# Kernel optimization log

Hardware: AMD Instinct MI355X
Metric: run time of the kernel (lower is better)

## Reference

```python
import jax, jax.numpy as jnp
import numpy as np

H = 32

def setup_inputs() -> dict:
    key = jax.random.key(0)
    ks = jax.random.split(key, 8)
    B, S = 256, 4096
    scale = 1.0 / np.sqrt(H)
    return {
        "lstm_outputs": jax.random.normal(ks[0], (B, S, H), dtype=jnp.float32),
        "final_hidden": jax.random.normal(ks[1], (B, H), dtype=jnp.float32),
        "Wq": jax.random.uniform(ks[2], (H, H), jnp.float32, -scale, scale),
        "bq": jax.random.uniform(ks[3], (H,), jnp.float32, -scale, scale),
        "Wk": jax.random.uniform(ks[4], (H, H), jnp.float32, -scale, scale),
        "bk": jax.random.uniform(ks[5], (H,), jnp.float32, -scale, scale),
        "Wv": jax.random.uniform(ks[6], (H, 1), jnp.float32, -scale, scale),
        "bv": jax.random.uniform(ks[7], (1,), jnp.float32, -scale, scale),
    }

def reference(lstm_outputs, final_hidden, Wq, bq, Wk, bk, Wv, bv):
    # keys: [B,S,H], query: [B,H]
    keys = jnp.einsum('bsh,hd->bsd', lstm_outputs, Wk) + bk
    query = final_hidden @ Wq + bq
    tanhed = jnp.tanh(query[:, None, :] + keys)            # [B,S,H]
    scores = jnp.einsum('bsh,h->bs', tanhed, Wv[:, 0]) + bv[0]  # [B,S]
    att_weights = jax.nn.softmax(scores, axis=-1)          # [B,S]
    context = jnp.einsum('bs,bsh->bh', att_weights, keys)  # [B,H]
    return context, att_weights
```

## Files before the change

kernel.cpp:

```cpp
#include <hip/hip_runtime.h>
#include <math.h>

#define HD 32
#define BB 256
#define SS 4096
#define BLK 256
#define POSB 256
#define NCH (SS / POSB)
#define PADW 40
#define PSTRIDE 33

typedef short bf16x8 __attribute__((ext_vector_type(8)));
typedef float f32x4 __attribute__((ext_vector_type(4)));

__device__ __forceinline__ float tanh_fast(float x) {
  float e = __builtin_amdgcn_exp2f(x * 2.8853900817779268f);
  return 1.0f - 2.0f * __builtin_amdgcn_rcpf(e + 1.0f);
}
__device__ __forceinline__ float exp_fast(float x) {
  return __builtin_amdgcn_exp2f(x * 1.4426950408889634f);
}
__device__ __forceinline__ short bf16_trunc(float x) {
  return (short)(__float_as_uint(x) >> 16);
}
__device__ __forceinline__ float hi_part(float x) {
  return __uint_as_float(__float_as_uint(x) & 0xffff0000u);
}
template <int CTRL>
__device__ __forceinline__ float dpp_ror(float x) {
  return __int_as_float(
      __builtin_amdgcn_update_dpp(0, __float_as_int(x), CTRL, 0xF, 0xF, true));
}

__global__ void __launch_bounds__(BLK, 4) bahdanau_p1(
    const float* __restrict__ lstm, const float* __restrict__ fh,
    const float* __restrict__ Wq, const float* __restrict__ bq,
    const float* __restrict__ Wk, const float* __restrict__ bk,
    const float* __restrict__ Wv, const float* __restrict__ bv,
    float* __restrict__ scores_out, float* __restrict__ partials) {
  __shared__ short sWkTh[HD * PADW];
  __shared__ short sWkTl[HD * PADW];
  __shared__ float sQB[HD];
  __shared__ float sWv[HD];
  __shared__ float sYp[4][HD];
  __shared__ float sRedL[4];

  const int tid = threadIdx.x;
  const int b = blockIdx.x >> 4;
  const int chunk = blockIdx.x & (NCH - 1);
  const int base = chunk * POSB;
  const int lane = tid & 63, w = tid >> 6;
  const int col = lane & 15, quad = lane >> 4;

  const float* gx = lstm + ((size_t)b * SS + base + w * 64) * HD;
  const float* rp = gx + (size_t)col * HD + quad * 8;
  float4 xa0 = ((const float4*)(rp + 0 * 16 * HD))[0];
  float4 xb0 = ((const float4*)(rp + 0 * 16 * HD))[1];
  float4 xa1 = ((const float4*)(rp + 1 * 16 * HD))[0];
  float4 xb1 = ((const float4*)(rp + 1 * 16 * HD))[1];
  float4 xa2 = ((const float4*)(rp + 2 * 16 * HD))[0];
  float4 xb2 = ((const float4*)(rp + 2 * 16 * HD))[1];
  float4 xa3 = ((const float4*)(rp + 3 * 16 * HD))[0];
  float4 xb3 = ((const float4*)(rp + 3 * 16 * HD))[1];

  {
    float4 w4 = ((const float4*)Wk)[tid];
    const int k = tid >> 3, h0 = (tid & 7) * 4;
    const float v[4] = {w4.x, w4.y, w4.z, w4.w};
#pragma unroll
    for (int i = 0; i < 4; i++) {
      const float hf = hi_part(v[i]);
      sWkTh[(h0 + i) * PADW + k] = bf16_trunc(v[i]);
      sWkTl[(h0 + i) * PADW + k] = bf16_trunc(v[i] - hf);
    }
  }
  if (tid < HD) {
    float acc = bq[tid] + bk[tid];
    const float* fhb = fh + b * HD;
#pragma unroll
    for (int j = 0; j < HD; j++) acc += fhb[j] * Wq[j * HD + tid];
    sQB[tid] = acc;
    sWv[tid] = Wv[tid];
  }
  __syncthreads();

  bf16x8 Bh0 = *(const bf16x8*)&sWkTh[(col)*PADW + quad * 8];
  bf16x8 Bl0 = *(const bf16x8*)&sWkTl[(col)*PADW + quad * 8];
  bf16x8 Bh1 = *(const bf16x8*)&sWkTh[(16 + col) * PADW + quad * 8];
  bf16x8 Bl1 = *(const bf16x8*)&sWkTl[(16 + col) * PADW + quad * 8];
  const float qb0 = sQB[col], qb1 = sQB[16 + col];
  const float wv0 = sWv[col], wv1 = sWv[16 + col];
  const float bv0 = bv[0];
  const int permLane = (col >> 2) * 16 + col;

  float lAcc = 0.f;
  float yp[8];
#pragma unroll
  for (int j = 0; j < 8; j++) yp[j] = 0.f;

#define MT_STEP(mt, XA, XB)                                                    \
  {                                                                            \
    const float xs[8] = {XA.x, XA.y, XA.z, XA.w, XB.x, XB.y, XB.z, XB.w};      \
    bf16x8 Ah, Al;                                                             \
    _Pragma("unroll") for (int j = 0; j < 8; j++) {                            \
      const float hf = hi_part(xs[j]);                                         \
      Ah[j] = bf16_trunc(xs[j]);                                               \
      Al[j] = bf16_trunc(xs[j] - hf);                                          \
    }                                                                          \
    f32x4 c0 = {0.f, 0.f, 0.f, 0.f}, c1 = {0.f, 0.f, 0.f, 0.f};                \
    c0 = __builtin_amdgcn_mfma_f32_16x16x32_bf16(Ah, Bh0, c0, 0, 0, 0);        \
    c1 = __builtin_amdgcn_mfma_f32_16x16x32_bf16(Ah, Bh1, c1, 0, 0, 0);        \
    c0 = __builtin_amdgcn_mfma_f32_16x16x32_bf16(Al, Bh0, c0, 0, 0, 0);        \
    c1 = __builtin_amdgcn_mfma_f32_16x16x32_bf16(Al, Bh1, c1, 0, 0, 0);        \
    c0 = __builtin_amdgcn_mfma_f32_16x16x32_bf16(Ah, Bl0, c0, 0, 0, 0);        \
    c1 = __builtin_amdgcn_mfma_f32_16x16x32_bf16(Ah, Bl1, c1, 0, 0, 0);        \
    float esc[4];                                                              \
    _Pragma("unroll") for (int r = 0; r < 4; r++) {                            \
      float t = tanh_fast(qb0 + c0[r]) * wv0 + tanh_fast(qb1 + c1[r]) * wv1;   \
      t += dpp_ror<0x128>(t);                                   \
      t += dpp_ror<0x124>(t);                                   \
      t += dpp_ror<0x122>(t);                                   \
      t += dpp_ror<0x121>(t);    \
      esc[r] = exp_fast(t + bv0);                                              \
    }                                                                          \
    const float s01 = (col & 1) ? esc[1] : esc[0];                             \
    const float s23 = (col & 1) ? esc[3] : esc[2];                             \
    const float sel = (col & 2) ? s23 : s01;        \
    const float e_m = __shfl(sel, permLane, 64);   \
    if (lane < 16)                                                             \
      scores_out[(size_t)b * SS + base + w * 64 + mt * 16 + lane] = e_m;       \
    lAcc += (lane < 16) ? e_m : 0.f;                                           \
    _Pragma("unroll") for (int j = 0; j < 8; j++)                              \
        yp[j] = fmaf(e_m, xs[j], yp[j]);                                       \
  }

  MT_STEP(0, xa0, xb0)
  MT_STEP(1, xa1, xb1)
  MT_STEP(2, xa2, xb2)
  MT_STEP(3, xa3, xb3)
#undef MT_STEP

#pragma unroll
  for (int j = 0; j < 8; j++) {
    yp[j] += __shfl_xor(yp[j], 1, 64);
    yp[j] += __shfl_xor(yp[j], 2, 64);
    yp[j] += __shfl_xor(yp[j], 4, 64);
    yp[j] += __shfl_xor(yp[j], 8, 64);
  }
  if (col == 0) {
#pragma unroll
    for (int j = 0; j < 8; j++) sYp[w][quad * 8 + j] = yp[j];
  }
#pragma unroll
  for (int off = 32; off >= 1; off >>= 1) lAcc += __shfl_xor(lAcc, off, 64);
  if (lane == 0) sRedL[w] = lAcc;
  __syncthreads();

  if (tid < HD) {
    float y = sYp[0][tid] + sYp[1][tid] + sYp[2][tid] + sYp[3][tid];
    float* p = partials + (size_t)blockIdx.x * PSTRIDE;
    p[1 + tid] = y;
    if (tid == 0) p[0] = sRedL[0] + sRedL[1] + sRedL[2] + sRedL[3];
  }
}

__global__ void __launch_bounds__(BLK) bahdanau_p2(
    const float* __restrict__ partials, const float* __restrict__ Wk,
    const float* __restrict__ bk, float* __restrict__ ctx_out,
    float* __restrict__ scores) {
  const int blk = blockIdx.x;
  const int b = blk >> 2;
  const int tid = threadIdx.x;
  __shared__ float sY[HD];

  float L = 0.f;
#pragma unroll
  for (int c = 0; c < NCH; c++)
    L += partials[(size_t)(b * NCH + c) * PSTRIDE];
  const float invL = __builtin_amdgcn_rcpf(L);

  if ((blk & 3) == 0) {
    if (tid < HD) {
      float y = 0.f;
#pragma unroll
      for (int c = 0; c < NCH; c++)
        y += partials[(size_t)(b * NCH + c) * PSTRIDE + 1 + tid];
      sY[tid] = y;
    }
    __syncthreads();
    if (tid < HD) {
      float cv = bk[tid] * L;
#pragma unroll
      for (int j = 0; j < HD; j++) cv = fmaf(sY[j], Wk[j * HD + tid], cv);
      ctx_out[b * HD + tid] = cv * invL;
    }
  }

  float4* srow = (float4*)(scores + (size_t)b * SS + (blk & 3) * 1024);
  float4 s = srow[tid];
  s.x *= invL; s.y *= invL; s.z *= invL; s.w *= invL;
  srow[tid] = s;
}

extern "C" void kernel_launch(void* const* d_in, const int* in_sizes, int n_in,
                              void* d_out, int out_size, void* d_ws,
                              size_t ws_size, hipStream_t stream) {
  const float* lstm = (const float*)d_in[0];
  const float* fh   = (const float*)d_in[1];
  const float* Wq   = (const float*)d_in[2];
  const float* bq   = (const float*)d_in[3];
  const float* Wk   = (const float*)d_in[4];
  const float* bk   = (const float*)d_in[5];
  const float* Wv   = (const float*)d_in[6];
  const float* bv   = (const float*)d_in[7];

  float* out = (float*)d_out;
  float* ctx_out = out;
  float* scores = out + BB * HD;
  float* partials = (float*)d_ws;

  bahdanau_p1<<<BB * NCH, BLK, 0, stream>>>(lstm, fh, Wq, bq, Wk, bk, Wv, bv,
                                            scores, partials);
  bahdanau_p2<<<BB * 4, BLK, 0, stream>>>(partials, Wk, bk, ctx_out, scores);
}
```

Before: 206.3 us.

## Hoist query/Wk split into prologue kernel, swap MFMA operands, per-wave partials

Adds a small prologue kernel that computes query+bias per batch and the bf16 hi/lo split of Wk once into workspace, so the main kernel no longer rebuilds them in LDS and needs no block barrier. The MFMA operands are swapped so that each lane holds per-position results over 4 hidden units. This lets the tanh/Wv reduction run as in-lane FMAs plus two cross-lane shuffles instead of DPP rotations and a permute shuffle. Each wave now writes its own partial record rather than reducing through shared memory, which makes the reduction kernel read 4x more partials. It also adds a third kernel launch.

Result: slower. 211.4 us (+2.4%).

```diff
diff --git a/kernel.cpp b/kernel.cpp
--- a/kernel.cpp
+++ b/kernel.cpp
@@ -7,8 +7,8 @@
 #define BLK 256
 #define POSB 256
 #define NCH (SS / POSB)
-#define PADW 40
-#define PSTRIDE 33
+#define NWREC 64
+#define PREC 36
 
 typedef short bf16x8 __attribute__((ext_vector_type(8)));
 typedef float f32x4 __attribute__((ext_vector_type(4)));
@@ -26,25 +26,39 @@
 __device__ __forceinline__ float hi_part(float x) {
   return __uint_as_float(__float_as_uint(x) & 0xffff0000u);
 }
-template <int CTRL>
-__device__ __forceinline__ float dpp_ror(float x) {
-  return __int_as_float(
-      __builtin_amdgcn_update_dpp(0, __float_as_int(x), CTRL, 0xF, 0xF, true));
+
+__global__ void __launch_bounds__(256) bahdanau_p0(
+    const float* __restrict__ fh, const float* __restrict__ Wq,
+    const float* __restrict__ bq, const float* __restrict__ bk,
+    const float* __restrict__ Wk, float* __restrict__ qbP,
+    short* __restrict__ wkH, short* __restrict__ wkL) {
+  const int tid = threadIdx.x;
+  if (blockIdx.x == 32) {
+    float4 w4 = ((const float4*)Wk)[tid];
+    const int k = tid >> 3, h0 = (tid & 7) * 4;
+    const float v[4] = {w4.x, w4.y, w4.z, w4.w};
+#pragma unroll
+    for (int i = 0; i < 4; i++) {
+      const float hf = hi_part(v[i]);
+      wkH[(h0 + i) * HD + k] = bf16_trunc(v[i]);
+      wkL[(h0 + i) * HD + k] = bf16_trunc(v[i] - hf);
+    }
+  } else {
+    const int b = blockIdx.x * 8 + (tid >> 5);
+    const int h = tid & 31;
+    float acc = bq[h] + bk[h];
+    const float* fhb = fh + b * HD;
+#pragma unroll
+    for (int j = 0; j < HD; j++) acc = fmaf(fhb[j], Wq[j * HD + h], acc);
+    qbP[b * HD + h] = acc;
+  }
 }
 
 __global__ void __launch_bounds__(BLK, 4) bahdanau_p1(
-    const float* __restrict__ lstm, const float* __restrict__ fh,
-    const float* __restrict__ Wq, const float* __restrict__ bq,
-    const float* __restrict__ Wk, const float* __restrict__ bk,
+    const float* __restrict__ lstm, const float* __restrict__ qbP,
+    const short* __restrict__ wkH, const short* __restrict__ wkL,
     const float* __restrict__ Wv, const float* __restrict__ bv,
     float* __restrict__ scores_out, float* __restrict__ partials) {
-  __shared__ short sWkTh[HD * PADW];
-  __shared__ short sWkTl[HD * PADW];
-  __shared__ float sQB[HD];
-  __shared__ float sWv[HD];
-  __shared__ float sYp[4][HD];
-  __shared__ float sRedL[4];
-
   const int tid = threadIdx.x;
   const int b = blockIdx.x >> 4;
   const int chunk = blockIdx.x & (NCH - 1);
@@ -52,8 +66,8 @@
   const int lane = tid & 63, w = tid >> 6;
   const int col = lane & 15, quad = lane >> 4;
 
-  const float* gx = lstm + ((size_t)b * SS + base + w * 64) * HD;
-  const float* rp = gx + (size_t)col * HD + quad * 8;
+  const float* rp =
+      lstm + ((size_t)b * SS + base + w * 64 + col) * HD + quad * 8;
   float4 xa0 = ((const float4*)(rp + 0 * 16 * HD))[0];
   float4 xb0 = ((const float4*)(rp + 0 * 16 * HD))[1];
   float4 xa1 = ((const float4*)(rp + 1 * 16 * HD))[0];
@@ -63,72 +77,51 @@
   float4 xa3 = ((const float4*)(rp + 3 * 16 * HD))[0];
   float4 xb3 = ((const float4*)(rp + 3 * 16 * HD))[1];
 
-  {
-    float4 w4 = ((const float4*)Wk)[tid];
-    const int k = tid >> 3, h0 = (tid & 7) * 4;
-    const float v[4] = {w4.x, w4.y, w4.z, w4.w};
-#pragma unroll
-    for (int i = 0; i < 4; i++) {
-      const float hf = hi_part(v[i]);
-      sWkTh[(h0 + i) * PADW + k] = bf16_trunc(v[i]);
-      sWkTl[(h0 + i) * PADW + k] = bf16_trunc(v[i] - hf);
-    }
-  }
-  if (tid < HD) {
-    float acc = bq[tid] + bk[tid];
-    const float* fhb = fh + b * HD;
-#pragma unroll
-    for (int j = 0; j < HD; j++) acc += fhb[j] * Wq[j * HD + tid];
-    sQB[tid] = acc;
-    sWv[tid] = Wv[tid];
-  }
-  __syncthreads();
-
-  bf16x8 Bh0 = *(const bf16x8*)&sWkTh[(col)*PADW + quad * 8];
-  bf16x8 Bl0 = *(const bf16x8*)&sWkTl[(col)*PADW + quad * 8];
-  bf16x8 Bh1 = *(const bf16x8*)&sWkTh[(16 + col) * PADW + quad * 8];
-  bf16x8 Bl1 = *(const bf16x8*)&sWkTl[(16 + col) * PADW + quad * 8];
-  const float qb0 = sQB[col], qb1 = sQB[16 + col];
-  const float wv0 = sWv[col], wv1 = sWv[16 + col];
+  const bf16x8 Ah0 = *(const bf16x8*)&wkH[col * HD + quad * 8];
+  const bf16x8 Al0 = *(const bf16x8*)&wkL[col * HD + quad * 8];
+  const bf16x8 Ah1 = *(const bf16x8*)&wkH[(16 + col) * HD + quad * 8];
+  const bf16x8 Al1 = *(const bf16x8*)&wkL[(16 + col) * HD + quad * 8];
+  const float4 qbA = ((const float4*)(qbP + b * HD))[quad];
+  const float4 qbB = ((const float4*)(qbP + b * HD))[quad + 4];
+  const float4 wvA = ((const float4*)Wv)[quad];
+  const float4 wvB = ((const float4*)Wv)[quad + 4];
   const float bv0 = bv[0];
-  const int permLane = (col >> 2) * 16 + col;
 
   float lAcc = 0.f;
   float yp[8];
 #pragma unroll
   for (int j = 0; j < 8; j++) yp[j] = 0.f;
+
+  const size_t srow = (size_t)b * SS + base;
 
 #define MT_STEP(mt, XA, XB)                                                    \
   {                                                                            \
     const float xs[8] = {XA.x, XA.y, XA.z, XA.w, XB.x, XB.y, XB.z, XB.w};      \
-    bf16x8 Ah, Al;                                                             \
+    bf16x8 Bh, Bl;                                                             \
     _Pragma("unroll") for (int j = 0; j < 8; j++) {                            \
       const float hf = hi_part(xs[j]);                                         \
-      Ah[j] = bf16_trunc(xs[j]);                                               \
-      Al[j] = bf16_trunc(xs[j] - hf);                                          \
+      Bh[j] = bf16_trunc(xs[j]);                                               \
+      Bl[j] = bf16_trunc(xs[j] - hf);                                          \
     }                                                                          \
     f32x4 c0 = {0.f, 0.f, 0.f, 0.f}, c1 = {0.f, 0.f, 0.f, 0.f};                \
-    c0 = __builtin_amdgcn_mfma_f32_16x16x32_bf16(Ah, Bh0, c0, 0, 0, 0);        \
-    c1 = __builtin_amdgcn_mfma_f32_16x16x32_bf16(Ah, Bh1, c1, 0, 0, 0);        \
-    c0 = __builtin_amdgcn_mfma_f32_16x16x32_bf16(Al, Bh0, c0, 0, 0, 0);        \
-    c1 = __builtin_amdgcn_mfma_f32_16x16x32_bf16(Al, Bh1, c1, 0, 0, 0);        \
-    c0 = __builtin_amdgcn_mfma_f32_16x16x32_bf16(Ah, Bl0, c0, 0, 0, 0);        \
-    c1 = __builtin_amdgcn_mfma_f32_16x16x32_bf16(Ah, Bl1, c1, 0, 0, 0);        \
-    float esc[4];                                                              \
-    _Pragma("unroll") for (int r = 0; r < 4; r++) {                            \
-      float t = tanh_fast(qb0 + c0[r]) * wv0 + tanh_fast(qb1 + c1[r]) * wv1;   \
-      t += dpp_ror<0x128>(t);                                   \
-      t += dpp_ror<0x124>(t);                                   \
-      t += dpp_ror<0x122>(t);                                   \
-      t += dpp_ror<0x121>(t);    \
-      esc[r] = exp_fast(t + bv0);                                              \
-    }                                                                          \
-    const float s01 = (col & 1) ? esc[1] : esc[0];                             \
-    const float s23 = (col & 1) ? esc[3] : esc[2];                             \
-    const float sel = (col & 2) ? s23 : s01;        \
-    const float e_m = __shfl(sel, permLane, 64);   \
-    if (lane < 16)                                                             \
-      scores_out[(size_t)b * SS + base + w * 64 + mt * 16 + lane] = e_m;       \
+    c0 = __builtin_amdgcn_mfma_f32_16x16x32_bf16(Ah0, Bh, c0, 0, 0, 0);        \
+    c1 = __builtin_amdgcn_mfma_f32_16x16x32_bf16(Ah1, Bh, c1, 0, 0, 0);        \
+    c0 = __builtin_amdgcn_mfma_f32_16x16x32_bf16(Al0, Bh, c0, 0, 0, 0);        \
+    c1 = __builtin_amdgcn_mfma_f32_16x16x32_bf16(Al1, Bh, c1, 0, 0, 0);        \
+    c0 = __builtin_amdgcn_mfma_f32_16x16x32_bf16(Ah0, Bl, c0, 0, 0, 0);        \
+    c1 = __builtin_amdgcn_mfma_f32_16x16x32_bf16(Ah1, Bl, c1, 0, 0, 0);        \
+    float t = tanh_fast(c0[0] + qbA.x) * wvA.x;                                \
+    t = fmaf(tanh_fast(c0[1] + qbA.y), wvA.y, t);                              \
+    t = fmaf(tanh_fast(c0[2] + qbA.z), wvA.z, t);                              \
+    t = fmaf(tanh_fast(c0[3] + qbA.w), wvA.w, t);                              \
+    t = fmaf(tanh_fast(c1[0] + qbB.x), wvB.x, t);                              \
+    t = fmaf(tanh_fast(c1[1] + qbB.y), wvB.y, t);                              \
+    t = fmaf(tanh_fast(c1[2] + qbB.z), wvB.z, t);                              \
+    t = fmaf(tanh_fast(c1[3] + qbB.w), wvB.w, t);                              \
+    t += __shfl_xor(t, 16, 64);                                                \
+    t += __shfl_xor(t, 32, 64);                                                \
+    const float e_m = exp_fast(t + bv0);     \
+    if (lane < 16) scores_out[srow + w * 64 + mt * 16 + lane] = e_m;           \
     lAcc += (lane < 16) ? e_m : 0.f;                                           \
     _Pragma("unroll") for (int j = 0; j < 8; j++)                              \
         yp[j] = fmaf(e_m, xs[j], yp[j]);                                       \
@@ -147,21 +140,19 @@
     yp[j] += __shfl_xor(yp[j], 4, 64);
     yp[j] += __shfl_xor(yp[j], 8, 64);
   }
+  lAcc += __shfl_xor(lAcc, 1, 64);
+  lAcc += __shfl_xor(lAcc, 2, 64);
+  lAcc += __shfl_xor(lAcc, 4, 64);
+  lAcc += __shfl_xor(lAcc, 8, 64);
+
+  float* rec = partials + (size_t)(blockIdx.x * 4 + w) * PREC;
   if (col == 0) {
-#pragma unroll
-    for (int j = 0; j < 8; j++) sYp[w][quad * 8 + j] = yp[j];
-  }
-#pragma unroll
-  for (int off = 32; off >= 1; off >>= 1) lAcc += __shfl_xor(lAcc, off, 64);
-  if (lane == 0) sRedL[w] = lAcc;
-  __syncthreads();
-
-  if (tid < HD) {
-    float y = sYp[0][tid] + sYp[1][tid] + sYp[2][tid] + sYp[3][tid];
-    float* p = partials + (size_t)blockIdx.x * PSTRIDE;
-    p[1 + tid] = y;
-    if (tid == 0) p[0] = sRedL[0] + sRedL[1] + sRedL[2] + sRedL[3];
-  }
+    const float4 y0 = {yp[0], yp[1], yp[2], yp[3]};
+    const float4 y1 = {yp[4], yp[5], yp[6], yp[7]};
+    ((float4*)(rec + 4))[quad * 2] = y0;
+    ((float4*)(rec + 4))[quad * 2 + 1] = y1;
+  }
+  if (lane == 0) rec[0] = lAcc;
 }
 
 __global__ void __launch_bounds__(BLK) bahdanau_p2(
@@ -174,17 +165,17 @@
   __shared__ float sY[HD];
 
   float L = 0.f;
-#pragma unroll
-  for (int c = 0; c < NCH; c++)
-    L += partials[(size_t)(b * NCH + c) * PSTRIDE];
+#pragma unroll 8
+  for (int c = 0; c < NWREC; c++)
+    L += partials[(size_t)(b * NWREC + c) * PREC];
   const float invL = __builtin_amdgcn_rcpf(L);
 
   if ((blk & 3) == 0) {
     if (tid < HD) {
       float y = 0.f;
-#pragma unroll
-      for (int c = 0; c < NCH; c++)
-        y += partials[(size_t)(b * NCH + c) * PSTRIDE + 1 + tid];
+#pragma unroll 8
+      for (int c = 0; c < NWREC; c++)
+        y += partials[(size_t)(b * NWREC + c) * PREC + 4 + tid];
       sY[tid] = y;
     }
     __syncthreads();
@@ -217,9 +208,14 @@
   float* out = (float*)d_out;
   float* ctx_out = out;
   float* scores = out + BB * HD;
+
   float* partials = (float*)d_ws;
-
-  bahdanau_p1<<<BB * NCH, BLK, 0, stream>>>(lstm, fh, Wq, bq, Wk, bk, Wv, bv,
+  short* wkH = (short*)((char*)d_ws + (size_t)BB * NWREC * PREC * 4);
+  short* wkL = wkH + HD * HD;
+  float* qbP = (float*)(wkL + HD * HD);
+
+  bahdanau_p0<<<33, 256, 0, stream>>>(fh, Wq, bq, bk, Wk, qbP, wkH, wkL);
+  bahdanau_p1<<<BB * NCH, BLK, 0, stream>>>(lstm, qbP, wkH, wkL, Wv, bv,
                                             scores, partials);
   bahdanau_p2<<<BB * 4, BLK, 0, stream>>>(partials, Wk, bk, ctx_out, scores);
 }
```
